# Optimization experiments

Measured on AMD Instinct MI355X. Metric: run time of the kernel, lower is better.

The kernel has to match this reference:

```python
import jax, jax.numpy as jnp
import numpy as np

B, N, E, D, H = 8, 5000, 160000, 64, 128  # batch, nodes, edges, gnn hidden, head hidden


def _w(key, shape, scale=0.05):
    return jax.random.normal(key, shape, jnp.float32) * scale


def setup_inputs() -> dict:
    key = jax.random.key(0)
    ks = jax.random.split(key, 24)
    inp = {
        "x": jax.random.normal(ks[0], (B, N), jnp.float32),
        "edges": jax.random.randint(ks[1], (E, 2), 0, N, dtype=jnp.int32),
        "emb": _w(ks[2], (N, D)),
        # conv1: prepare FFN (2 layers, no bias, elu), update FFN (2 layers, bias)
        "c1_pw1": _w(ks[3], (D, D)), "c1_pw2": _w(ks[4], (D, D)),
        "c1_uw1": _w(ks[5], (2 * D, D)), "c1_ub1": jnp.zeros((D,), jnp.float32),
        "c1_uw2": _w(ks[6], (D, D)), "c1_ub2": jnp.zeros((D,), jnp.float32),
        # conv2
        "c2_pw1": _w(ks[7], (D, D)), "c2_pw2": _w(ks[8], (D, D)),
        "c2_uw1": _w(ks[9], (2 * D, D)), "c2_ub1": jnp.zeros((D,), jnp.float32),
        "c2_uw2": _w(ks[10], (D, D)), "c2_ub2": jnp.zeros((D,), jnp.float32),
        # TARnet prob heads: flatten -> Dense(H, elu) -> Dense(2) (mu, log_sigma)
        "w0a": _w(ks[11], (N * D, H), 0.005), "b0a": jnp.zeros((H,), jnp.float32),
        "w0b": _w(ks[12], (H, 2)), "b0b": jnp.zeros((2,), jnp.float32),
        "w1a": _w(ks[13], (N * D, H), 0.005), "b1a": jnp.zeros((H,), jnp.float32),
        "w1b": _w(ks[14], (H, 2)), "b1b": jnp.zeros((2,), jnp.float32),
    }
    return inp


def _graph_conv(h, edges, pw1, pw2, uw1, ub1, uw2, ub2):
    # h: [B, N, D]; edges: [E, 2] (parent, node)
    parents = jnp.take(h, edges[:, 0], axis=1)            # [B, E, D] gather
    m = jax.nn.elu(parents @ pw1)                          # prepare FFN (no bias)
    m = jax.nn.elu(m @ pw2)
    agg = jnp.zeros_like(h).at[:, edges[:, 1]].add(m)      # unsorted_segment_sum -> [B, N, D]
    hcat = jnp.concatenate([h, agg], axis=-1)              # combination_type='concat'
    u = jax.nn.elu(hcat @ uw1 + ub1)                       # update FFN
    return u @ uw2 + ub2                                   # final_activation=None


def reference(x, edges, emb,
              c1_pw1, c1_pw2, c1_uw1, c1_ub1, c1_uw2, c1_ub2,
              c2_pw1, c2_pw2, c2_uw1, c2_ub1, c2_uw2, c2_ub2,
              w0a, b0a, w0b, b0b, w1a, b1a, w1b, b1b):
    # node features scale learned per-node embeddings -> [B, N, D]
    h = x[:, :, None] * emb[None, :, :]
    h = _graph_conv(h, edges, c1_pw1, c1_pw2, c1_uw1, c1_ub1, c1_uw2, c1_ub2)
    h = _graph_conv(h, edges, c2_pw1, c2_pw2, c2_uw1, c2_ub1, c2_uw2, c2_ub2)
    phi = h.reshape(h.shape[0], -1)                        # flatten [B, N*D]
    y0 = jax.nn.elu(phi @ w0a + b0a) @ w0b + b0b           # [B, 2] (mu, log_sigma)
    y1 = jax.nn.elu(phi @ w1a + b1a) @ w1b + b1b           # [B, 2]
    return jnp.concatenate([y0, y1], axis=1)               # [B, 4]
```

## Files before the change

kernel.cpp:

```cpp
#include <hip/hip_runtime.h>


constexpr int B = 8, N = 5000, E = 160000, D = 64, H = 128;
constexpr int BN = B * N;
constexpr int ND = N * D;
constexpr long BND = (long)BN * D;
constexpr int KC = 320;
constexpr int NIT = KC / 8;
constexpr int XB = ND / KC;

using f32x4 = __attribute__((ext_vector_type(4))) float;

__device__ __forceinline__ float elu_f(float x) {
    return x > 0.0f ? x : __expf(x) - 1.0f;
}

__device__ __forceinline__ void g2lds16(const float* g, float* l) {
    __builtin_amdgcn_global_load_lds(
        (const __attribute__((address_space(1))) void*)g,
        (__attribute__((address_space(3))) void*)l, 16, 0, 0);
}

__global__ __launch_bounds__(256) void k_count(const int* __restrict__ edges,
                                               int* __restrict__ cnt) {
    int i = blockIdx.x * 256 + threadIdx.x;
    if (i < E) atomicAdd(&cnt[edges[2 * i + 1]], 1);
}

__global__ __launch_bounds__(256) void k_scan(const int* __restrict__ cnt,
                                              int* __restrict__ offs) {
    __shared__ int part[256];
    int t = threadIdx.x;
    const int CH = 20;
    int base = t * CH;
    int s = 0;
    for (int i = 0; i < CH; ++i) { int idx = base + i; if (idx < N) s += cnt[idx]; }
    part[t] = s;
    __syncthreads();
    for (int off = 1; off < 256; off <<= 1) {
        int add = (t >= off) ? part[t - off] : 0;
        __syncthreads();
        part[t] += add;
        __syncthreads();
    }
    int run = part[t] - s;
    for (int i = 0; i < CH; ++i) {
        int idx = base + i;
        if (idx < N) { offs[idx] = run; run += cnt[idx]; }
    }
    if (t == 255) offs[N] = run;
}

__global__ __launch_bounds__(256) void k_fill(const int* __restrict__ edges,
                                              const int* __restrict__ offs,
                                              int* __restrict__ cursor,
                                              int* __restrict__ elist) {
    int i = blockIdx.x * 256 + threadIdx.x;
    if (i < E) {
        int child = edges[2 * i + 1];
        int pos = offs[child] + atomicAdd(&cursor[child], 1);
        elist[pos] = edges[2 * i];
    }
}

__global__ __launch_bounds__(512) void k_prepare(const float* __restrict__ xsrc,
                                                 const float* __restrict__ emb,
                                                 const float* __restrict__ W1,
                                                 const float* __restrict__ W2,
                                                 float* __restrict__ M,
                                                 float* __restrict__ hwt) {
    __shared__ float sW1[64 * 64];
    __shared__ float sP[128 * 65];
    int t = threadIdx.x;
    int r0 = blockIdx.x * 128;
    for (int i = t; i < 4096; i += 512) sW1[i] = W1[i];
    for (int i = t; i < 128 * 64; i += 512) {
        int r = i >> 6, c = i & 63;
        int row = r0 + r;
        float v = 0.0f;
        if (row < BN) {
            int n = row % N;
            v = xsrc[row] * emb[n * 64 + c];
            hwt[(long)row * 64 + c] = v;
        }
        sP[r * 65 + c] = v;
    }
    __syncthreads();

    int cg = t & 15, rg = t >> 4;
    float acc[4][4] = {};
    #pragma unroll 4
    for (int k = 0; k < 64; ++k) {
        float a[4];
        #pragma unroll
        for (int i = 0; i < 4; ++i) a[i] = sP[(rg * 4 + i) * 65 + k];
        float4 bb = *reinterpret_cast<const float4*>(&sW1[k * 64 + cg * 4]);
        #pragma unroll
        for (int i = 0; i < 4; ++i) {
            acc[i][0] += a[i] * bb.x; acc[i][1] += a[i] * bb.y;
            acc[i][2] += a[i] * bb.z; acc[i][3] += a[i] * bb.w;
        }
    }
    __syncthreads();
    #pragma unroll
    for (int i = 0; i < 4; ++i)
        #pragma unroll
        for (int j = 0; j < 4; ++j)
            sP[(rg * 4 + i) * 65 + cg * 4 + j] = elu_f(acc[i][j]);
    __syncthreads();

    float acc2[4][4] = {};
    #pragma unroll 4
    for (int k = 0; k < 64; ++k) {
        float a[4];
        #pragma unroll
        for (int i = 0; i < 4; ++i) a[i] = sP[(rg * 4 + i) * 65 + k];
        float4 bb = *reinterpret_cast<const float4*>(&W2[k * 64 + cg * 4]);
        #pragma unroll
        for (int i = 0; i < 4; ++i) {
            acc2[i][0] += a[i] * bb.x; acc2[i][1] += a[i] * bb.y;
            acc2[i][2] += a[i] * bb.z; acc2[i][3] += a[i] * bb.w;
        }
    }
    #pragma unroll
    for (int i = 0; i < 4; ++i) {
        int row = r0 + rg * 4 + i;
        if (row < BN) {
            int b = row / N;
            int n = row - b * N;
            float4 o = make_float4(elu_f(acc2[i][0]), elu_f(acc2[i][1]),
                                   elu_f(acc2[i][2]), elu_f(acc2[i][3]));
            *reinterpret_cast<float4*>(&M[((long)n * 8 + b) * 64 + cg * 4]) = o;
        }
    }
}

template <int PREP>
__global__ __launch_bounds__(512, 8) void k_conv(const float* __restrict__ h,
                                                 const float* __restrict__ M,
                                                 const int* __restrict__ offs,
                                                 const int* __restrict__ elist,
                                                 const float* __restrict__ W1u,
                                                 const float* __restrict__ b1u,
                                                 const float* __restrict__ W2u,
                                                 const float* __restrict__ b2u,
                                                 float* __restrict__ hout,
                                                 const float* __restrict__ W1p,
                                                 const float* __restrict__ W2p,
                                                 float* __restrict__ Mout) {
    __shared__ float sP[64 * 129];
    int t = threadIdx.x;
    int n0 = blockIdx.x * 8;

    #pragma unroll
    for (int q = 0; q < 2; ++q) {
        int s = t + q * 512;
        int lr = s >> 4, c4 = s & 15;
        int nl = lr >> 3, b = lr & 7;
        long grow = (long)b * N + (n0 + nl);
        float4 v = *reinterpret_cast<const float4*>(&h[grow * 64 + c4 * 4]);
        int base = lr * 129 + c4 * 4;
        sP[base + 0] = v.x; sP[base + 1] = v.y;
        sP[base + 2] = v.z; sP[base + 3] = v.w;
    }
    {
        int wv = t >> 6, l = t & 63;
        int n = n0 + wv;
        int e0 = __builtin_amdgcn_readfirstlane(offs[n]);
        int e1 = __builtin_amdgcn_readfirstlane(offs[n + 1]);
        float4 a1 = make_float4(0.f, 0.f, 0.f, 0.f);
        float4 a2 = make_float4(0.f, 0.f, 0.f, 0.f);
        float4 a3 = make_float4(0.f, 0.f, 0.f, 0.f);
        float4 a4 = make_float4(0.f, 0.f, 0.f, 0.f);
        int e = e0;
        for (; e + 1 < e1; e += 2) {
            int p1 = elist[e], p2 = elist[e + 1];
            const float4* q1 = reinterpret_cast<const float4*>(M + (long)p1 * 512);
            const float4* q2 = reinterpret_cast<const float4*>(M + (long)p2 * 512);
            float4 v1 = q1[l], v2 = q1[64 + l];
            float4 v3 = q2[l], v4 = q2[64 + l];
            a1.x += v1.x; a1.y += v1.y; a1.z += v1.z; a1.w += v1.w;
            a2.x += v2.x; a2.y += v2.y; a2.z += v2.z; a2.w += v2.w;
            a3.x += v3.x; a3.y += v3.y; a3.z += v3.z; a3.w += v3.w;
            a4.x += v4.x; a4.y += v4.y; a4.z += v4.z; a4.w += v4.w;
        }
        if (e < e1) {
            int p = elist[e];
            const float4* q = reinterpret_cast<const float4*>(M + (long)p * 512);
            float4 v1 = q[l], v2 = q[64 + l];
            a1.x += v1.x; a1.y += v1.y; a1.z += v1.z; a1.w += v1.w;
            a2.x += v2.x; a2.y += v2.y; a2.z += v2.z; a2.w += v2.w;
        }
        a1.x += a3.x; a1.y += a3.y; a1.z += a3.z; a1.w += a3.w;
        a2.x += a4.x; a2.y += a4.y; a2.z += a4.z; a2.w += a4.w;
        int c4 = l & 15, br = l >> 4;
        int base1 = (wv * 8 + br) * 129 + 64 + c4 * 4;
        int base2 = (wv * 8 + 4 + br) * 129 + 64 + c4 * 4;
        sP[base1 + 0] = a1.x; sP[base1 + 1] = a1.y;
        sP[base1 + 2] = a1.z; sP[base1 + 3] = a1.w;
        sP[base2 + 0] = a2.x; sP[base2 + 1] = a2.y;
        sP[base2 + 2] = a2.z; sP[base2 + 3] = a2.w;
    }
    __syncthreads();

    int cg = t & 15, rg = t >> 4;
    float acc[2][4] = {};
    #pragma unroll 4
    for (int k = 0; k < 128; ++k) {
        float a0 = sP[(rg * 2 + 0) * 129 + k];
        float a1 = sP[(rg * 2 + 1) * 129 + k];
        float4 bb = *reinterpret_cast<const float4*>(&W1u[k * 64 + cg * 4]);
        acc[0][0] += a0 * bb.x; acc[0][1] += a0 * bb.y; acc[0][2] += a0 * bb.z; acc[0][3] += a0 * bb.w;
        acc[1][0] += a1 * bb.x; acc[1][1] += a1 * bb.y; acc[1][2] += a1 * bb.z; acc[1][3] += a1 * bb.w;
    }
    float4 bv1 = *reinterpret_cast<const float4*>(&b1u[cg * 4]);
    __syncthreads();
    #pragma unroll
    for (int i = 0; i < 2; ++i) {
        int base = (rg * 2 + i) * 129 + cg * 4;
        sP[base + 0] = elu_f(acc[i][0] + bv1.x);
        sP[base + 1] = elu_f(acc[i][1] + bv1.y);
        sP[base + 2] = elu_f(acc[i][2] + bv1.z);
        sP[base + 3] = elu_f(acc[i][3] + bv1.w);
    }
    __syncthreads();

    float acc2[2][4] = {};
    #pragma unroll 4
    for (int k = 0; k < 64; ++k) {
        float a0 = sP[(rg * 2 + 0) * 129 + k];
        float a1 = sP[(rg * 2 + 1) * 129 + k];
        float4 bb = *reinterpret_cast<const float4*>(&W2u[k * 64 + cg * 4]);
        acc2[0][0] += a0 * bb.x; acc2[0][1] += a0 * bb.y; acc2[0][2] += a0 * bb.z; acc2[0][3] += a0 * bb.w;
        acc2[1][0] += a1 * bb.x; acc2[1][1] += a1 * bb.y; acc2[1][2] += a1 * bb.z; acc2[1][3] += a1 * bb.w;
    }
    float4 bv2 = *reinterpret_cast<const float4*>(&b2u[cg * 4]);
    #pragma unroll
    for (int i = 0; i < 2; ++i) {
        int lr = rg * 2 + i;
        int nl = lr >> 3, b = lr & 7;
        float4 o = make_float4(acc2[i][0] + bv2.x, acc2[i][1] + bv2.y,
                               acc2[i][2] + bv2.z, acc2[i][3] + bv2.w);
        *reinterpret_cast<float4*>(
            &hout[((long)b * N + (n0 + nl)) * 64 + cg * 4]) = o;
        if (PREP) {
            int base = lr * 129 + 64 + cg * 4;
            sP[base + 0] = o.x; sP[base + 1] = o.y;
            sP[base + 2] = o.z; sP[base + 3] = o.w;
        }
    }

    if (PREP) {
        __syncthreads();
        float acc3[2][4] = {};
        #pragma unroll 4
        for (int k = 0; k < 64; ++k) {
            float a0 = sP[(rg * 2 + 0) * 129 + 64 + k];
            float a1 = sP[(rg * 2 + 1) * 129 + 64 + k];
            float4 bb = *reinterpret_cast<const float4*>(&W1p[k * 64 + cg * 4]);
            acc3[0][0] += a0 * bb.x; acc3[0][1] += a0 * bb.y; acc3[0][2] += a0 * bb.z; acc3[0][3] += a0 * bb.w;
            acc3[1][0] += a1 * bb.x; acc3[1][1] += a1 * bb.y; acc3[1][2] += a1 * bb.z; acc3[1][3] += a1 * bb.w;
        }
        #pragma unroll
        for (int i = 0; i < 2; ++i) {
            int base = (rg * 2 + i) * 129 + cg * 4;
            sP[base + 0] = elu_f(acc3[i][0]);
            sP[base + 1] = elu_f(acc3[i][1]);
            sP[base + 2] = elu_f(acc3[i][2]);
            sP[base + 3] = elu_f(acc3[i][3]);
        }
        __syncthreads();
        float acc4[2][4] = {};
        #pragma unroll 4
        for (int k = 0; k < 64; ++k) {
            float a0 = sP[(rg * 2 + 0) * 129 + k];
            float a1 = sP[(rg * 2 + 1) * 129 + k];
            float4 bb = *reinterpret_cast<const float4*>(&W2p[k * 64 + cg * 4]);
            acc4[0][0] += a0 * bb.x; acc4[0][1] += a0 * bb.y; acc4[0][2] += a0 * bb.z; acc4[0][3] += a0 * bb.w;
            acc4[1][0] += a1 * bb.x; acc4[1][1] += a1 * bb.y; acc4[1][2] += a1 * bb.z; acc4[1][3] += a1 * bb.w;
        }
        #pragma unroll
        for (int i = 0; i < 2; ++i) {
            int lr = rg * 2 + i;
            int nl = lr >> 3, b = lr & 7;
            float4 o = make_float4(elu_f(acc4[i][0]), elu_f(acc4[i][1]),
                                   elu_f(acc4[i][2]), elu_f(acc4[i][3]));
            *reinterpret_cast<float4*>(
                &Mout[((long)(n0 + nl) * 8 + b) * 64 + cg * 4]) = o;
        }
    }
}

__global__ __launch_bounds__(256) void k_head(const float* __restrict__ phi,
                                              const float* __restrict__ wa,
                                              float* __restrict__ part) {
    __shared__ float smem[4 * 32 * 33];
    __shared__ __align__(16) float wb[8][1024];
    int t = threadIdx.x;
    int k0 = blockIdx.x * KC;

    #pragma unroll
    for (int b = 0; b < 8; ++b)
        for (int kk = t; kk < KC; kk += 256)
            smem[b * KC + kk] = phi[(long)b * ND + k0 + kk];
    __syncthreads();

    int w = t >> 6, l = t & 63;
    int h4 = l & 31, kh = l >> 5;
    int kl = w * 2 + kh;
    const float* wp = wa + (long)(k0 + kl) * H + h4 * 4;

    float4 acc[8];
    #pragma unroll
    for (int b = 0; b < 8; ++b) acc[b] = make_float4(0.f, 0.f, 0.f, 0.f);

    unsigned my_off =
        (unsigned)(size_t)(__attribute__((address_space(3))) float*)&wb[0][0]
        + (unsigned)t * 16u;

    const float* wq = wp;
    #pragma unroll
    for (int j = 0; j < 8; ++j) {
        g2lds16(wq, &wb[j][w * 256]);
        wq += 8 * H;
    }

#define STEP(I, CNT, OFF, RE)                                              \
    {                                                                      \
        asm volatile("s_waitcnt vmcnt(" #CNT ")" ::: "memory");            \
        __builtin_amdgcn_sched_barrier(0);                                 \
        f32x4 w4;                                                          \
        asm volatile("ds_read_b128 %0, %1 offset:" #OFF                    \
                     : "=v"(w4) : "v"(my_off));                            \
        float pv[8];                                                       \
        _Pragma("unroll")                                                  \
        for (int b = 0; b < 8; ++b)                                        \
            pv[b] = smem[b * KC + (I) * 8 + kl];                           \
        asm volatile("s_waitcnt lgkmcnt(0)" ::: "memory");                 \
        __builtin_amdgcn_sched_barrier(0);                                 \
        _Pragma("unroll")                                                  \
        for (int b = 0; b < 8; ++b) {                                      \
            acc[b].x += pv[b] * w4.x; acc[b].y += pv[b] * w4.y;            \
            acc[b].z += pv[b] * w4.z; acc[b].w += pv[b] * w4.w;            \
        }                                                                  \
        if (RE) {                                                          \
            g2lds16(wq, &wb[(I) & 7][w * 256]);                            \
            wq += 8 * H;                                                   \
        }                                                                  \
    }

#define ROUND8(BASE, RE)                                                   \
    STEP(BASE + 0, 7, 0,     RE) STEP(BASE + 1, 7, 4096,  RE)              \
    STEP(BASE + 2, 7, 8192,  RE) STEP(BASE + 3, 7, 12288, RE)              \
    STEP(BASE + 4, 7, 16384, RE) STEP(BASE + 5, 7, 20480, RE)              \
    STEP(BASE + 6, 7, 24576, RE) STEP(BASE + 7, 7, 28672, RE)

    ROUND8(0, 1) ROUND8(8, 1) ROUND8(16, 1) ROUND8(24, 1)
    STEP(32, 7, 0,     0) STEP(33, 6, 4096,  0)
    STEP(34, 5, 8192,  0) STEP(35, 4, 12288, 0)
    STEP(36, 3, 16384, 0) STEP(37, 2, 20480, 0)
    STEP(38, 1, 24576, 0) STEP(39, 0, 28672, 0)
#undef ROUND8
#undef STEP

    #pragma unroll
    for (int b = 0; b < 8; ++b) {
        acc[b].x += __shfl_xor(acc[b].x, 32);
        acc[b].y += __shfl_xor(acc[b].y, 32);
        acc[b].z += __shfl_xor(acc[b].z, 32);
        acc[b].w += __shfl_xor(acc[b].w, 32);
    }
    __syncthreads();
    if (kh == 0) {
        int base = (w * 32 + h4) * 33;
        #pragma unroll
        for (int b = 0; b < 8; ++b) {
            smem[base + b * 4 + 0] = acc[b].x;
            smem[base + b * 4 + 1] = acc[b].y;
            smem[base + b * 4 + 2] = acc[b].z;
            smem[base + b * 4 + 3] = acc[b].w;
        }
    }
    __syncthreads();

    int h4r = t & 31, br = t >> 5;
    float s0 = 0.f, s1 = 0.f, s2 = 0.f, s3 = 0.f;
    #pragma unroll
    for (int wv = 0; wv < 4; ++wv) {
        int idx = (wv * 32 + h4r) * 33 + br * 4;
        s0 += smem[idx + 0]; s1 += smem[idx + 1];
        s2 += smem[idx + 2]; s3 += smem[idx + 3];
    }
    float* pb = part + (long)blockIdx.x * 1024;
    *reinterpret_cast<float4*>(&pb[br * H + h4r * 4]) =
        make_float4(s0, s1, s2, s3);
}

__global__ __launch_bounds__(256) void k_reduce(const float* __restrict__ part,
                                                float* __restrict__ hidden) {
    int idx = blockIdx.x * 256 + threadIdx.x;
    int c = blockIdx.y;
    int y = idx >> 10, j = idx & 1023;
    const float* p = part + (long)y * XB * 1024 + j;
    int x0 = (XB * c) >> 4, x1 = (XB * (c + 1)) >> 4;
    float s0 = 0.f, s1 = 0.f, s2 = 0.f, s3 = 0.f;
    int x = x0;
    for (; x + 3 < x1; x += 4) {
        s0 += p[(long)(x + 0) * 1024];
        s1 += p[(long)(x + 1) * 1024];
        s2 += p[(long)(x + 2) * 1024];
        s3 += p[(long)(x + 3) * 1024];
    }
    for (; x < x1; ++x) s0 += p[(long)x * 1024];
    unsafeAtomicAdd(&hidden[y * 1024 + j], s0 + s1 + s2 + s3);
}

__global__ __launch_bounds__(64) void k_final(const float* __restrict__ hidden,
                                              const float* __restrict__ b0a,
                                              const float* __restrict__ w0b,
                                              const float* __restrict__ b0b,
                                              const float* __restrict__ b1a,
                                              const float* __restrict__ w1b,
                                              const float* __restrict__ b1b,
                                              float* __restrict__ out) {
    int t = threadIdx.x;
    if (t >= 32) return;
    int head = t >> 4, b = (t >> 1) & 7, j = t & 1;
    const float* hid = hidden + head * (8 * H) + b * H;
    const float* ba = head ? b1a : b0a;
    const float* wb = head ? w1b : w0b;
    const float* bb = head ? b1b : b0b;
    float acc = 0.0f;
    for (int hh = 0; hh < H; ++hh)
        acc += elu_f(hid[hh] + ba[hh]) * wb[hh * 2 + j];
    out[b * 4 + head * 2 + j] = acc + bb[j];
}

extern "C" void kernel_launch(void* const* d_in, const int* in_sizes, int n_in,
                              void* d_out, int out_size, void* d_ws, size_t ws_size,
                              hipStream_t stream) {
    const float* x      = (const float*)d_in[0];
    const int*   edges  = (const int*)d_in[1];
    const float* emb    = (const float*)d_in[2];
    const float* c1_pw1 = (const float*)d_in[3];
    const float* c1_pw2 = (const float*)d_in[4];
    const float* c1_uw1 = (const float*)d_in[5];
    const float* c1_ub1 = (const float*)d_in[6];
    const float* c1_uw2 = (const float*)d_in[7];
    const float* c1_ub2 = (const float*)d_in[8];
    const float* c2_pw1 = (const float*)d_in[9];
    const float* c2_pw2 = (const float*)d_in[10];
    const float* c2_uw1 = (const float*)d_in[11];
    const float* c2_ub1 = (const float*)d_in[12];
    const float* c2_uw2 = (const float*)d_in[13];
    const float* c2_ub2 = (const float*)d_in[14];
    const float* w0a    = (const float*)d_in[15];
    const float* b0a    = (const float*)d_in[16];
    const float* w0b    = (const float*)d_in[17];
    const float* b0b    = (const float*)d_in[18];
    const float* w1a    = (const float*)d_in[19];
    const float* b1a    = (const float*)d_in[20];
    const float* w1b    = (const float*)d_in[21];
    const float* b1b    = (const float*)d_in[22];
    float* out = (float*)d_out;

    float* hA     = (float*)d_ws;
    float* hB     = hA + BND;
    float* Mu     = hB + BND;
    float* M2     = Mu + BND;
    float* hidden = M2 + BND;
    int* cnt      = (int*)(hidden + 2048);
    int* cursor   = cnt + N;
    int* offs     = cursor + N;
    int* elist    = offs + N + 1;
    float* part   = Mu;

    hipMemsetAsync(hidden, 0, (2048 + 2 * N) * sizeof(float), stream);

    k_count<<<(E + 255) / 256, 256, 0, stream>>>(edges, cnt);
    k_scan<<<1, 256, 0, stream>>>(cnt, offs);
    k_fill<<<(E + 255) / 256, 256, 0, stream>>>(edges, offs, cursor, elist);

    k_prepare<<<(BN + 127) / 128, 512, 0, stream>>>(x, emb, c1_pw1, c1_pw2, Mu, hA);
    k_conv<1><<<N / 8, 512, 0, stream>>>(hA, Mu, offs, elist,
                                         c1_uw1, c1_ub1, c1_uw2, c1_ub2, hB,
                                         c2_pw1, c2_pw2, M2);
    k_conv<0><<<N / 8, 512, 0, stream>>>(hB, M2, offs, elist,
                                         c2_uw1, c2_ub1, c2_uw2, c2_ub2, hA,
                                         nullptr, nullptr, nullptr);

    k_head<<<XB, 256, 0, stream>>>(hA, w0a, part);
    k_head<<<XB, 256, 0, stream>>>(hA, w1a, part + (long)XB * 1024);
    k_reduce<<<dim3(8, 16), 256, 0, stream>>>(part, hidden);
    k_final<<<1, 64, 0, stream>>>(hidden, b0a, w0b, b0b, b1a, w1b, b1b, out);
}
```

Before: 626.7 us.

## Fuse edge counting into prepare, recompute input in conv, merge head launches

Edge-degree counting moves into k_prepare, so the separate k_count launch goes away. k_prepare no longer writes the initial h tensor; the first conv recomputes x*emb on the fly instead, which removes a full B*N*D store and reload. The two head kernels become one launch with a 2D grid. The atomic reduction into hidden is replaced by per-chunk partial stores that k_final sums, which also lets the memset shrink. Together these cut launch count and global traffic, at the cost of slightly more work in k_final and atomics inside k_prepare.

New measurement: 655.4 us (median of 2 runs). 4.6% more time.

```diff
diff --git a/kernel.cpp b/kernel.cpp
--- a/kernel.cpp
+++ b/kernel.cpp
@@ -19,12 +19,6 @@
     __builtin_amdgcn_global_load_lds(
         (const __attribute__((address_space(1))) void*)g,
         (__attribute__((address_space(3))) void*)l, 16, 0, 0);
-}
-
-__global__ __launch_bounds__(256) void k_count(const int* __restrict__ edges,
-                                               int* __restrict__ cnt) {
-    int i = blockIdx.x * 256 + threadIdx.x;
-    if (i < E) atomicAdd(&cnt[edges[2 * i + 1]], 1);
 }
 
 __global__ __launch_bounds__(256) void k_scan(const int* __restrict__ cnt,
@@ -65,14 +59,19 @@
 
 __global__ __launch_bounds__(512) void k_prepare(const float* __restrict__ xsrc,
                                                  const float* __restrict__ emb,
+                                                 const int* __restrict__ edges,
+                                                 int* __restrict__ cnt,
                                                  const float* __restrict__ W1,
                                                  const float* __restrict__ W2,
-                                                 float* __restrict__ M,
-                                                 float* __restrict__ hwt) {
+                                                 float* __restrict__ M) {
     __shared__ float sW1[64 * 64];
     __shared__ float sP[128 * 65];
     int t = threadIdx.x;
     int r0 = blockIdx.x * 128;
+    {
+        int i = blockIdx.x * 512 + t;
+        if (i < E) atomicAdd(&cnt[edges[2 * i + 1]], 1);
+    }
     for (int i = t; i < 4096; i += 512) sW1[i] = W1[i];
     for (int i = t; i < 128 * 64; i += 512) {
         int r = i >> 6, c = i & 63;
@@ -81,7 +80,6 @@
         if (row < BN) {
             int n = row % N;
             v = xsrc[row] * emb[n * 64 + c];
-            hwt[(long)row * 64 + c] = v;
         }
         sP[r * 65 + c] = v;
     }
@@ -137,6 +135,8 @@
 
 template <int PREP>
 __global__ __launch_bounds__(512, 8) void k_conv(const float* __restrict__ h,
+                                                 const float* __restrict__ xsrc,
+                                                 const float* __restrict__ emb,
                                                  const float* __restrict__ M,
                                                  const int* __restrict__ offs,
                                                  const int* __restrict__ elist,
@@ -158,7 +158,15 @@
         int lr = s >> 4, c4 = s & 15;
         int nl = lr >> 3, b = lr & 7;
         long grow = (long)b * N + (n0 + nl);
-        float4 v = *reinterpret_cast<const float4*>(&h[grow * 64 + c4 * 4]);
+        float4 v;
+        if (PREP) {
+            float xv = xsrc[grow];
+            float4 ev = *reinterpret_cast<const float4*>(
+                &emb[(long)(n0 + nl) * 64 + c4 * 4]);
+            v = make_float4(xv * ev.x, xv * ev.y, xv * ev.z, xv * ev.w);
+        } else {
+            v = *reinterpret_cast<const float4*>(&h[grow * 64 + c4 * 4]);
+        }
         int base = lr * 129 + c4 * 4;
         sP[base + 0] = v.x; sP[base + 1] = v.y;
         sP[base + 2] = v.z; sP[base + 3] = v.w;
@@ -292,10 +300,12 @@
 }
 
 __global__ __launch_bounds__(256) void k_head(const float* __restrict__ phi,
-                                              const float* __restrict__ wa,
+                                              const float* __restrict__ w0a,
+                                              const float* __restrict__ w1a,
                                               float* __restrict__ part) {
     __shared__ float smem[4 * 32 * 33];
     __shared__ __align__(16) float wb[8][1024];
+    const float* wa = blockIdx.y ? w1a : w0a;
     int t = threadIdx.x;
     int k0 = blockIdx.x * KC;
 
@@ -391,13 +401,13 @@
         s0 += smem[idx + 0]; s1 += smem[idx + 1];
         s2 += smem[idx + 2]; s3 += smem[idx + 3];
     }
-    float* pb = part + (long)blockIdx.x * 1024;
+    float* pb = part + ((long)blockIdx.y * XB + blockIdx.x) * 1024;
     *reinterpret_cast<float4*>(&pb[br * H + h4r * 4]) =
         make_float4(s0, s1, s2, s3);
 }
 
 __global__ __launch_bounds__(256) void k_reduce(const float* __restrict__ part,
-                                                float* __restrict__ hidden) {
+                                                float* __restrict__ hidden2) {
     int idx = blockIdx.x * 256 + threadIdx.x;
     int c = blockIdx.y;
     int y = idx >> 10, j = idx & 1023;
@@ -412,10 +422,10 @@
         s3 += p[(long)(x + 3) * 1024];
     }
     for (; x < x1; ++x) s0 += p[(long)x * 1024];
-    unsafeAtomicAdd(&hidden[y * 1024 + j], s0 + s1 + s2 + s3);
-}
-
-__global__ __launch_bounds__(64) void k_final(const float* __restrict__ hidden,
+    hidden2[c * 2048 + idx] = s0 + s1 + s2 + s3;
+}
+
+__global__ __launch_bounds__(64) void k_final(const float* __restrict__ hidden2,
                                               const float* __restrict__ b0a,
                                               const float* __restrict__ w0b,
                                               const float* __restrict__ b0b,
@@ -426,13 +436,17 @@
     int t = threadIdx.x;
     if (t >= 32) return;
     int head = t >> 4, b = (t >> 1) & 7, j = t & 1;
-    const float* hid = hidden + head * (8 * H) + b * H;
+    int base = head * 1024 + b * H;
     const float* ba = head ? b1a : b0a;
     const float* wb = head ? w1b : w0b;
     const float* bb = head ? b1b : b0b;
     float acc = 0.0f;
-    for (int hh = 0; hh < H; ++hh)
-        acc += elu_f(hid[hh] + ba[hh]) * wb[hh * 2 + j];
+    for (int hh = 0; hh < H; ++hh) {
+        float hv = 0.0f;
+        #pragma unroll
+        for (int c = 0; c < 16; ++c) hv += hidden2[c * 2048 + base + hh];
+        acc += elu_f(hv + ba[hh]) * wb[hh * 2 + j];
+    }
     out[b * 4 + head * 2 + j] = acc + bb[j];
 }
 
@@ -464,33 +478,29 @@
     const float* b1b    = (const float*)d_in[22];
     float* out = (float*)d_out;
 
-    float* hA     = (float*)d_ws;
-    float* hB     = hA + BND;
-    float* Mu     = hB + BND;
-    float* M2     = Mu + BND;
-    float* hidden = M2 + BND;
-    int* cnt      = (int*)(hidden + 2048);
-    int* cursor   = cnt + N;
-    int* offs     = cursor + N;
-    int* elist    = offs + N + 1;
-    float* part   = Mu;
-
-    hipMemsetAsync(hidden, 0, (2048 + 2 * N) * sizeof(float), stream);
-
-    k_count<<<(E + 255) / 256, 256, 0, stream>>>(edges, cnt);
+    float* hA      = (float*)d_ws;
+    float* hB      = hA + BND;
+    float* Mu      = hB + BND;
+    float* M2      = Mu + BND;
+    float* hidden2 = M2 + BND;
+    int* cnt       = (int*)(hidden2 + 32768);
+    int* cursor    = cnt + N;
+    int* offs      = cursor + N;
+    int* elist     = offs + N + 1;
+    float* part    = Mu;
+
+    hipMemsetAsync(cnt, 0, 2 * N * sizeof(int), stream);
+    k_prepare<<<(BN + 127) / 128, 512, 0, stream>>>(x, emb, edges, cnt,
+                                                    c1_pw1, c1_pw2, Mu);
     k_scan<<<1, 256, 0, stream>>>(cnt, offs);
     k_fill<<<(E + 255) / 256, 256, 0, stream>>>(edges, offs, cursor, elist);
-
-    k_prepare<<<(BN + 127) / 128, 512, 0, stream>>>(x, emb, c1_pw1, c1_pw2, Mu, hA);
-    k_conv<1><<<N / 8, 512, 0, stream>>>(hA, Mu, offs, elist,
+    k_conv<1><<<N / 8, 512, 0, stream>>>(nullptr, x, emb, Mu, offs, elist,
                                          c1_uw1, c1_ub1, c1_uw2, c1_ub2, hB,
                                          c2_pw1, c2_pw2, M2);
-    k_conv<0><<<N / 8, 512, 0, stream>>>(hB, M2, offs, elist,
+    k_conv<0><<<N / 8, 512, 0, stream>>>(hB, nullptr, nullptr, M2, offs, elist,
                                          c2_uw1, c2_ub1, c2_uw2, c2_ub2, hA,
                                          nullptr, nullptr, nullptr);
-
-    k_head<<<XB, 256, 0, stream>>>(hA, w0a, part);
-    k_head<<<XB, 256, 0, stream>>>(hA, w1a, part + (long)XB * 1024);
-    k_reduce<<<dim3(8, 16), 256, 0, stream>>>(part, hidden);
-    k_final<<<1, 64, 0, stream>>>(hidden, b0a, w0b, b0b, b1a, w1b, b1b, out);
-}
+    k_head<<<dim3(XB, 2), 256, 0, stream>>>(hA, w0a, w1a, part);
+    k_reduce<<<dim3(8, 16), 256, 0, stream>>>(part, hidden2);
+    k_final<<<1, 64, 0, stream>>>(hidden2, b0a, w0b, b0b, b1a, w1b, b1b, out);
+}
```
